# Kernel tuning notes

Hardware: AMD Instinct MI355X
Metric: run time of the kernel (lower is better)

The kernel has to match this reference:

```python
import jax, jax.numpy as jnp
import numpy as np

C, C_LO, C_MF = 96, 32, 32  # c_hf = 96 - 32 - 32 = 32
K_LO, K_HI, LP_FINE, LP_COARSE = 5, 3, 3, 7
BN_EPS = 1e-5


def _avgpool_same(x, k):
    """AvgPool2d(k, stride=1, padding=k//2, count_include_pad=False) on NCHW."""
    p = k // 2
    dims, strides = (1, 1, k, k), (1, 1, 1, 1)
    pads = ((0, 0), (0, 0), (p, p), (p, p))
    s = jax.lax.reduce_window(x, jnp.float32(0), jax.lax.add, dims, strides, pads)
    ones = jnp.ones((1, 1) + x.shape[2:], x.dtype)
    cnt = jax.lax.reduce_window(ones, jnp.float32(0), jax.lax.add, dims, strides, pads)
    return s / cnt  # divide by number of VALID (non-pad) elements


def _dwconv(x, w, k):
    """Depthwise conv, 'same' padding, no bias. w: (C, 1, k, k)."""
    p = k // 2
    return jax.lax.conv_general_dilated(
        x, w, window_strides=(1, 1), padding=((p, p), (p, p)),
        dimension_numbers=("NCHW", "OIHW", "NCHW"),
        feature_group_count=x.shape[1])


def setup_inputs() -> dict:
    key = jax.random.key(0)
    ks = jax.random.split(key, 8)
    B, H, W = 8, 256, 256
    return {
        "x": jax.random.normal(ks[0], (B, C, H, W), jnp.float32),
        "w_lo": jax.random.normal(ks[1], (C_LO, 1, K_LO, K_LO), jnp.float32) * 0.1,
        "w_mf": jax.random.normal(ks[2], (C_MF, 1, 3, 3), jnp.float32) * 0.2,
        "w_hf": jax.random.normal(ks[3], (C - C_LO - C_MF, 1, K_HI, K_HI), jnp.float32) * 0.2,
        "bn_gamma": jax.random.uniform(ks[4], (C,), jnp.float32, 0.5, 1.5),
        "bn_beta": jax.random.normal(ks[5], (C,), jnp.float32) * 0.1,
        "bn_mean": jax.random.normal(ks[6], (C,), jnp.float32) * 0.1,
        "bn_var": jax.random.uniform(ks[7], (C,), jnp.float32, 0.5, 1.5),
    }


def reference(x, w_lo, w_mf, w_hf, bn_gamma, bn_beta, bn_mean, bn_var):
    x_lo = x[:, :C_LO]
    x_mf = x[:, C_LO:C_LO + C_MF]
    x_hf = x[:, C_LO + C_MF:]

    y_lo = _dwconv(x_lo, w_lo, K_LO)
    # band-pass: fine low-pass minus coarse low-pass
    x_mf_bp = _avgpool_same(x_mf, LP_FINE) - _avgpool_same(x_mf, LP_COARSE)
    y_mf = _dwconv(x_mf_bp, w_mf, 3)
    # high-pass: identity minus fine low-pass
    x_hf_hp = x_hf - _avgpool_same(x_hf, LP_FINE)
    y_hf = _dwconv(x_hf_hp, w_hf, K_HI)

    y = jnp.concatenate([y_lo, y_mf, y_hf], axis=1)

    # channel shuffle with groups=3 (C % 3 == 0 here)
    B, Cc, H, W = y.shape
    y = y.reshape(B, 3, Cc // 3, H, W).transpose(0, 2, 1, 3, 4).reshape(B, Cc, H, W)

    # BatchNorm2d (inference mode, running stats) + SiLU
    inv = bn_gamma * jax.lax.rsqrt(bn_var + BN_EPS)
    y = y * inv[None, :, None, None] + (bn_beta - bn_mean * inv)[None, :, None, None]
    return jax.nn.silu(y)
```

## Files before the change

kernel.cpp:

```cpp
#include <hip/hip_runtime.h>

#define HH 256
#define WW 256
#define CC 96
#define BB 8

__device__ __forceinline__ float silu_of(float z) {
    return z / (1.0f + __expf(-z));
}

__global__ __launch_bounds__(256, 4)
void trifreq_kernel(const float* __restrict__ x,
                    const float* __restrict__ w_lo,
                    const float* __restrict__ w_mf,
                    const float* __restrict__ w_hf,
                    const float* __restrict__ gamma,
                    const float* __restrict__ beta,
                    const float* __restrict__ mean,
                    const float* __restrict__ var,
                    float* __restrict__ out)
{
    __shared__ __align__(16) float xs[74 * 72 + 16];
    __shared__ __align__(16) float tmp[36 * 68];

    const int tid = threadIdx.x;
    const int tileIdx = blockIdx.x;
    const int c = blockIdx.y;
    const int b = blockIdx.z;
    const int th = (tileIdx >> 2) * 64;
    const int tw = (tileIdx & 3) * 64;

    const int g = c >> 5;
    const int ci = c & 31;
    const int c_out = ci * 3 + g;

    const float* __restrict__ xin = x + (((size_t)b * CC + c) * (size_t)HH) * (size_t)WW;

    for (int idx = tid; idx < 72 * 18; idx += 256) {
        const int r  = idx / 18;
        const int c4 = idx % 18;
        const int gh = th - 4 + r;
        const int gw = tw - 4 + 4 * c4;
        float4 v = make_float4(0.f, 0.f, 0.f, 0.f);
        if (gh >= 0 && gh < HH && gw >= 0 && gw + 3 < WW) {
            v = *reinterpret_cast<const float4*>(xin + (size_t)gh * WW + gw);
        }
        *reinterpret_cast<float4*>(&xs[r * 72 + 4 * c4]) = v;
    }
    __syncthreads();

    if (g == 0) {
        const int qr = (tid >> 4) << 2;
        const int qc = (tid & 15) << 2;
        const float* __restrict__ wp = w_lo + ci * 25;
        float wk[25];
        #pragma unroll
        for (int t = 0; t < 25; ++t) wk[t] = wp[t];
        float acc[4][4];
        #pragma unroll
        for (int i = 0; i < 4; ++i)
            #pragma unroll
            for (int j = 0; j < 4; ++j) acc[i][j] = 0.f;

        #pragma unroll
        for (int rr = 0; rr < 8; ++rr) {
            const float* row = &xs[(qr + rr + 2) * 72 + qc];
            float v[12];
            *reinterpret_cast<float4*>(&v[0]) = *reinterpret_cast<const float4*>(row);
            *reinterpret_cast<float4*>(&v[4]) = *reinterpret_cast<const float4*>(row + 4);
            *reinterpret_cast<float4*>(&v[8]) = *reinterpret_cast<const float4*>(row + 8);
            #pragma unroll
            for (int i = 0; i < 4; ++i) {
                const int ki = rr - i;
                if (ki >= 0 && ki < 5) {
                    #pragma unroll
                    for (int j = 0; j < 4; ++j)
                        acc[i][j] += v[j + 2] * wk[ki * 5 + 0]
                                   + v[j + 3] * wk[ki * 5 + 1]
                                   + v[j + 4] * wk[ki * 5 + 2]
                                   + v[j + 5] * wk[ki * 5 + 3]
                                   + v[j + 6] * wk[ki * 5 + 4];
                }
            }
        }

        const float bninv  = gamma[c_out] * rsqrtf(var[c_out] + 1e-5f);
        const float bnbias = beta[c_out] - mean[c_out] * bninv;
        float* __restrict__ op = out + (((size_t)b * CC + c_out) * (size_t)HH + (th + qr)) * (size_t)WW + (tw + qc);
        #pragma unroll
        for (int i = 0; i < 4; ++i) {
            float4 o;
            o.x = silu_of(acc[i][0] * bninv + bnbias);
            o.y = silu_of(acc[i][1] * bninv + bnbias);
            o.z = silu_of(acc[i][2] * bninv + bnbias);
            o.w = silu_of(acc[i][3] * bninv + bnbias);
            *reinterpret_cast<float4*>(op + (size_t)i * WW) = o;
        }
    } else {
        for (int c0 = 0; c0 < 2; ++c0) {
            const int R0 = c0 * 32 - 1;

            if (tid < 153) {
                int pr, pc;
                if (tid < 144) { pr = tid >> 4; pc = tid & 15; }
                else           { pr = tid - 144; pc = 16; }
                const int bc = pc * 4 - 1;
                const int hb = th + R0 + pr * 4;
                const int wb = tw + bc;

                if (g == 1) {
                    const int xrb = R0 + 1 + pr * 4;
                    float v7a[4][4] = {};
                    float v3a[4][4] = {};
                    #pragma unroll
                    for (int rr = 0; rr < 10; ++rr) {
                        const float* row = &xs[(xrb + rr) * 72 + pc * 4];
                        float v[12];
                        *reinterpret_cast<float4*>(&v[0]) = *reinterpret_cast<const float4*>(row);
                        *reinterpret_cast<float4*>(&v[4]) = *reinterpret_cast<const float4*>(row + 4);
                        *reinterpret_cast<float4*>(&v[8]) = *reinterpret_cast<const float4*>(row + 8);
                        float h7[4], h3[4];
                        float s = v[0] + v[1] + v[2] + v[3] + v[4] + v[5] + v[6];
                        h7[0] = s;
                        h7[1] = h7[0] + v[7] - v[0];
                        h7[2] = h7[1] + v[8] - v[1];
                        h7[3] = h7[2] + v[9] - v[2];
                        #pragma unroll
                        for (int j = 0; j < 4; ++j) h3[j] = v[j + 2] + v[j + 3] + v[j + 4];
                        #pragma unroll
                        for (int k = 0; k < 4; ++k) {
                            if (rr >= k && rr <= k + 6) {
                                #pragma unroll
                                for (int j = 0; j < 4; ++j) v7a[k][j] += h7[j];
                            }
                            if (rr >= k + 2 && rr <= k + 4) {
                                #pragma unroll
                                for (int j = 0; j < 4; ++j) v3a[k][j] += h3[j];
                            }
                        }
                    }
                    float r3h[4], r7h[4], r3w[4], r7w[4];
                    if (hb >= 3 && hb + 6 <= HH - 1) {
                        #pragma unroll
                        for (int i = 0; i < 4; ++i) { r3h[i] = (1.f / 3.f); r7h[i] = (1.f / 7.f); }
                    } else {
                        #pragma unroll
                        for (int i = 0; i < 4; ++i) {
                            const int hh = hb + i;
                            const int a3 = min(hh + 1, HH - 1) - max(hh - 1, 0) + 1;
                            const int a7 = min(hh + 3, HH - 1) - max(hh - 3, 0) + 1;
                            r3h[i] = 1.0f / (float)a3;
                            r7h[i] = 1.0f / (float)a7;
                        }
                    }
                    if (wb >= 3 && wb + 6 <= WW - 1) {
                        #pragma unroll
                        for (int j = 0; j < 4; ++j) { r3w[j] = (1.f / 3.f); r7w[j] = (1.f / 7.f); }
                    } else {
                        #pragma unroll
                        for (int j = 0; j < 4; ++j) {
                            const int ww = wb + j;
                            const int a3 = min(ww + 1, WW - 1) - max(ww - 1, 0) + 1;
                            const int a7 = min(ww + 3, WW - 1) - max(ww - 3, 0) + 1;
                            r3w[j] = 1.0f / (float)a3;
                            r7w[j] = 1.0f / (float)a7;
                        }
                    }
                    #pragma unroll
                    for (int i = 0; i < 4; ++i) {
                        const int hh = hb + i;
                        float bpv[4];
                        #pragma unroll
                        for (int j = 0; j < 4; ++j) {
                            const int ww = wb + j;
                            float bp = 0.f;
                            if (hh >= 0 && hh < HH && ww >= 0 && ww < WW)
                                bp = v3a[i][j] * (r3h[i] * r3w[j]) - v7a[i][j] * (r7h[i] * r7w[j]);
                            bpv[j] = bp;
                        }
                        *reinterpret_cast<float4*>(&tmp[(pr * 4 + i) * 68 + pc * 4]) =
                            make_float4(bpv[0], bpv[1], bpv[2], bpv[3]);
                    }
                } else {
                    const int xrb = R0 + 3 + pr * 4;
                    float v3a[4][4] = {};
                    float cen[4][4];
                    #pragma unroll
                    for (int rr = 0; rr < 6; ++rr) {
                        const float* row = &xs[(xrb + rr) * 72 + pc * 4];
                        float v[8];
                        *reinterpret_cast<float4*>(&v[0]) = *reinterpret_cast<const float4*>(row);
                        *reinterpret_cast<float4*>(&v[4]) = *reinterpret_cast<const float4*>(row + 4);
                        float h3[4];
                        #pragma unroll
                        for (int j = 0; j < 4; ++j) h3[j] = v[j + 2] + v[j + 3] + v[j + 4];
                        if (rr >= 1 && rr <= 4) {
                            #pragma unroll
                            for (int j = 0; j < 4; ++j) cen[rr - 1][j] = v[j + 3];
                        }
                        #pragma unroll
                        for (int k = 0; k < 4; ++k) {
                            if (rr >= k && rr <= k + 2) {
                                #pragma unroll
                                for (int j = 0; j < 4; ++j) v3a[k][j] += h3[j];
                            }
                        }
                    }
                    float r3h[4], r3w[4];
                    if (hb >= 1 && hb + 4 <= HH - 1) {
                        #pragma unroll
                        for (int i = 0; i < 4; ++i) r3h[i] = (1.f / 3.f);
                    } else {
                        #pragma unroll
                        for (int i = 0; i < 4; ++i) {
                            const int hh = hb + i;
                            const int a3 = min(hh + 1, HH - 1) - max(hh - 1, 0) + 1;
                            r3h[i] = 1.0f / (float)a3;
                        }
                    }
                    if (wb >= 1 && wb + 4 <= WW - 1) {
                        #pragma unroll
                        for (int j = 0; j < 4; ++j) r3w[j] = (1.f / 3.f);
                    } else {
                        #pragma unroll
                        for (int j = 0; j < 4; ++j) {
                            const int ww = wb + j;
                            const int a3 = min(ww + 1, WW - 1) - max(ww - 1, 0) + 1;
                            r3w[j] = 1.0f / (float)a3;
                        }
                    }
                    #pragma unroll
                    for (int i = 0; i < 4; ++i) {
                        const int hh = hb + i;
                        float hpv[4];
                        #pragma unroll
                        for (int j = 0; j < 4; ++j) {
                            const int ww = wb + j;
                            float hp = 0.f;
                            if (hh >= 0 && hh < HH && ww >= 0 && ww < WW)
                                hp = cen[i][j] - v3a[i][j] * (r3h[i] * r3w[j]);
                            hpv[j] = hp;
                        }
                        *reinterpret_cast<float4*>(&tmp[(pr * 4 + i) * 68 + pc * 4]) =
                            make_float4(hpv[0], hpv[1], hpv[2], hpv[3]);
                    }
                }
            }
            __syncthreads();

            const float* __restrict__ wp = ((g == 1) ? w_mf : w_hf) + ci * 9;
            float wk[9];
            #pragma unroll
            for (int t = 0; t < 9; ++t) wk[t] = wp[t];

            const int lqr = (tid >> 4) * 2;
            const int qc  = (tid & 15) * 4;
            float acc2[2][4];
            #pragma unroll
            for (int i = 0; i < 2; ++i)
                #pragma unroll
                for (int j = 0; j < 4; ++j) acc2[i][j] = 0.f;

            #pragma unroll
            for (int rr = 0; rr < 4; ++rr) {
                const float* row = &tmp[(lqr + rr) * 68 + qc];
                float v[8];
                *reinterpret_cast<float4*>(&v[0]) = *reinterpret_cast<const float4*>(row);
                *reinterpret_cast<float4*>(&v[4]) = *reinterpret_cast<const float4*>(row + 4);
                #pragma unroll
                for (int i = 0; i < 2; ++i) {
                    const int ki = rr - i;
                    if (ki >= 0 && ki < 3) {
                        #pragma unroll
                        for (int j = 0; j < 4; ++j)
                            acc2[i][j] += v[j + 0] * wk[ki * 3 + 0]
                                        + v[j + 1] * wk[ki * 3 + 1]
                                        + v[j + 2] * wk[ki * 3 + 2];
                    }
                }
            }

            const float bninv  = gamma[c_out] * rsqrtf(var[c_out] + 1e-5f);
            const float bnbias = beta[c_out] - mean[c_out] * bninv;
            float* __restrict__ op = out + (((size_t)b * CC + c_out) * (size_t)HH
                                            + (th + c0 * 32 + lqr)) * (size_t)WW + (tw + qc);
            #pragma unroll
            for (int i = 0; i < 2; ++i) {
                float4 o;
                o.x = silu_of(acc2[i][0] * bninv + bnbias);
                o.y = silu_of(acc2[i][1] * bninv + bnbias);
                o.z = silu_of(acc2[i][2] * bninv + bnbias);
                o.w = silu_of(acc2[i][3] * bninv + bnbias);
                *reinterpret_cast<float4*>(op + (size_t)i * WW) = o;
            }

            if (c0 == 0) __syncthreads();
        }
    }
}

extern "C" void kernel_launch(void* const* d_in, const int* in_sizes, int n_in,
                              void* d_out, int out_size, void* d_ws, size_t ws_size,
                              hipStream_t stream) {
    const float* x     = (const float*)d_in[0];
    const float* w_lo  = (const float*)d_in[1];
    const float* w_mf  = (const float*)d_in[2];
    const float* w_hf  = (const float*)d_in[3];
    const float* gam   = (const float*)d_in[4];
    const float* bet   = (const float*)d_in[5];
    const float* mea   = (const float*)d_in[6];
    const float* va    = (const float*)d_in[7];
    float* out = (float*)d_out;

    dim3 grid(16, CC, BB);
    dim3 block(256);
    hipLaunchKernelGGL(trifreq_kernel, grid, block, 0, stream,
                       x, w_lo, w_mf, w_hf, gam, bet, mea, va, out);
}
```

Measured before the change: 420.1 us.

## Store filtered intermediate tile as fp16 and process full 64-row tile in one pass

The band-pass and high-pass intermediate tile is now stored in shared memory as half precision. The saved space allows the whole 66x66 prefilter region to be held at once, so the two half-tile passes with their extra barrier and halo recomputation are replaced by a single pass. The 3x3 conv and the BN+SiLU epilogue are unified with the low-band path using 4x4 outputs per thread. The fp16 rounding of intermediates adds numerical error, and the prefilter loop is now strided over 289 work items.

```diff
diff --git a/kernel.cpp b/kernel.cpp
--- a/kernel.cpp
+++ b/kernel.cpp
@@ -1,4 +1,5 @@
 #include <hip/hip_runtime.h>
+#include <hip/hip_fp16.h>
 
 #define HH 256
 #define WW 256
@@ -21,7 +22,7 @@
                     float* __restrict__ out)
 {
     __shared__ __align__(16) float xs[74 * 72 + 16];
-    __shared__ __align__(16) float tmp[36 * 68];
+    __shared__ __align__(16) __half tmp[68 * 68 + 8];
 
     const int tid = threadIdx.x;
     const int tileIdx = blockIdx.x;
@@ -49,14 +50,15 @@
     }
     __syncthreads();
 
+    const int qr = (tid >> 4) << 2;
+    const int qc = (tid & 15) << 2;
+    float acc[4][4];
+
     if (g == 0) {
-        const int qr = (tid >> 4) << 2;
-        const int qc = (tid & 15) << 2;
         const float* __restrict__ wp = w_lo + ci * 25;
         float wk[25];
         #pragma unroll
         for (int t = 0; t < 25; ++t) wk[t] = wp[t];
-        float acc[4][4];
         #pragma unroll
         for (int i = 0; i < 4; ++i)
             #pragma unroll
@@ -83,219 +85,200 @@
                 }
             }
         }
-
-        const float bninv  = gamma[c_out] * rsqrtf(var[c_out] + 1e-5f);
-        const float bnbias = beta[c_out] - mean[c_out] * bninv;
-        float* __restrict__ op = out + (((size_t)b * CC + c_out) * (size_t)HH + (th + qr)) * (size_t)WW + (tw + qc);
-        #pragma unroll
-        for (int i = 0; i < 4; ++i) {
-            float4 o;
-            o.x = silu_of(acc[i][0] * bninv + bnbias);
-            o.y = silu_of(acc[i][1] * bninv + bnbias);
-            o.z = silu_of(acc[i][2] * bninv + bnbias);
-            o.w = silu_of(acc[i][3] * bninv + bnbias);
-            *reinterpret_cast<float4*>(op + (size_t)i * WW) = o;
-        }
     } else {
-        for (int c0 = 0; c0 < 2; ++c0) {
-            const int R0 = c0 * 32 - 1;
-
-            if (tid < 153) {
-                int pr, pc;
-                if (tid < 144) { pr = tid >> 4; pc = tid & 15; }
-                else           { pr = tid - 144; pc = 16; }
-                const int bc = pc * 4 - 1;
-                const int hb = th + R0 + pr * 4;
+        if (g == 1) {
+            for (int p = tid; p < 17 * 17; p += 256) {
+                const int pr = p / 17, pc = p % 17;
+                const int br = pr * 4 - 1, bc = pc * 4 - 1;
+                const int hb = th + br;
                 const int wb = tw + bc;
-
-                if (g == 1) {
-                    const int xrb = R0 + 1 + pr * 4;
-                    float v7a[4][4] = {};
-                    float v3a[4][4] = {};
-                    #pragma unroll
-                    for (int rr = 0; rr < 10; ++rr) {
-                        const float* row = &xs[(xrb + rr) * 72 + pc * 4];
-                        float v[12];
-                        *reinterpret_cast<float4*>(&v[0]) = *reinterpret_cast<const float4*>(row);
-                        *reinterpret_cast<float4*>(&v[4]) = *reinterpret_cast<const float4*>(row + 4);
-                        *reinterpret_cast<float4*>(&v[8]) = *reinterpret_cast<const float4*>(row + 8);
-                        float h7[4], h3[4];
-                        float s = v[0] + v[1] + v[2] + v[3] + v[4] + v[5] + v[6];
-                        h7[0] = s;
-                        h7[1] = h7[0] + v[7] - v[0];
-                        h7[2] = h7[1] + v[8] - v[1];
-                        h7[3] = h7[2] + v[9] - v[2];
-                        #pragma unroll
-                        for (int j = 0; j < 4; ++j) h3[j] = v[j + 2] + v[j + 3] + v[j + 4];
-                        #pragma unroll
-                        for (int k = 0; k < 4; ++k) {
-                            if (rr >= k && rr <= k + 6) {
-                                #pragma unroll
-                                for (int j = 0; j < 4; ++j) v7a[k][j] += h7[j];
-                            }
-                            if (rr >= k + 2 && rr <= k + 4) {
-                                #pragma unroll
-                                for (int j = 0; j < 4; ++j) v3a[k][j] += h3[j];
-                            }
+                float v7a[4][4] = {};
+                float v3a[4][4] = {};
+                #pragma unroll
+                for (int rr = 0; rr < 10; ++rr) {
+                    const float* row = &xs[(pr * 4 + rr) * 72 + pc * 4];
+                    float v[12];
+                    *reinterpret_cast<float4*>(&v[0]) = *reinterpret_cast<const float4*>(row);
+                    *reinterpret_cast<float4*>(&v[4]) = *reinterpret_cast<const float4*>(row + 4);
+                    *reinterpret_cast<float4*>(&v[8]) = *reinterpret_cast<const float4*>(row + 8);
+                    float h7[4], h3[4];
+                    float s = v[0] + v[1] + v[2] + v[3] + v[4] + v[5] + v[6];
+                    h7[0] = s;
+                    h7[1] = h7[0] + v[7] - v[0];
+                    h7[2] = h7[1] + v[8] - v[1];
+                    h7[3] = h7[2] + v[9] - v[2];
+                    #pragma unroll
+                    for (int j = 0; j < 4; ++j) h3[j] = v[j + 2] + v[j + 3] + v[j + 4];
+                    #pragma unroll
+                    for (int k = 0; k < 4; ++k) {
+                        if (rr >= k && rr <= k + 6) {
+                            #pragma unroll
+                            for (int j = 0; j < 4; ++j) v7a[k][j] += h7[j];
                         }
-                    }
-                    float r3h[4], r7h[4], r3w[4], r7w[4];
-                    if (hb >= 3 && hb + 6 <= HH - 1) {
-                        #pragma unroll
-                        for (int i = 0; i < 4; ++i) { r3h[i] = (1.f / 3.f); r7h[i] = (1.f / 7.f); }
-                    } else {
-                        #pragma unroll
-                        for (int i = 0; i < 4; ++i) {
-                            const int hh = hb + i;
-                            const int a3 = min(hh + 1, HH - 1) - max(hh - 1, 0) + 1;
-                            const int a7 = min(hh + 3, HH - 1) - max(hh - 3, 0) + 1;
-                            r3h[i] = 1.0f / (float)a3;
-                            r7h[i] = 1.0f / (float)a7;
+                        if (rr >= k + 2 && rr <= k + 4) {
+                            #pragma unroll
+                            for (int j = 0; j < 4; ++j) v3a[k][j] += h3[j];
                         }
                     }
-                    if (wb >= 3 && wb + 6 <= WW - 1) {
-                        #pragma unroll
-                        for (int j = 0; j < 4; ++j) { r3w[j] = (1.f / 3.f); r7w[j] = (1.f / 7.f); }
-                    } else {
-                        #pragma unroll
-                        for (int j = 0; j < 4; ++j) {
-                            const int ww = wb + j;
-                            const int a3 = min(ww + 1, WW - 1) - max(ww - 1, 0) + 1;
-                            const int a7 = min(ww + 3, WW - 1) - max(ww - 3, 0) + 1;
-                            r3w[j] = 1.0f / (float)a3;
-                            r7w[j] = 1.0f / (float)a7;
-                        }
-                    }
+                }
+                float r3h[4], r7h[4], r3w[4], r7w[4];
+                if (hb >= 3 && hb + 6 <= HH - 1) {
+                    #pragma unroll
+                    for (int i = 0; i < 4; ++i) { r3h[i] = (1.f / 3.f); r7h[i] = (1.f / 7.f); }
+                } else {
                     #pragma unroll
                     for (int i = 0; i < 4; ++i) {
                         const int hh = hb + i;
-                        float bpv[4];
+                        const int a3 = min(hh + 1, HH - 1) - max(hh - 1, 0) + 1;
+                        const int a7 = min(hh + 3, HH - 1) - max(hh - 3, 0) + 1;
+                        r3h[i] = 1.0f / (float)a3;
+                        r7h[i] = 1.0f / (float)a7;
+                    }
+                }
+                if (wb >= 3 && wb + 6 <= WW - 1) {
+                    #pragma unroll
+                    for (int j = 0; j < 4; ++j) { r3w[j] = (1.f / 3.f); r7w[j] = (1.f / 7.f); }
+                } else {
+                    #pragma unroll
+                    for (int j = 0; j < 4; ++j) {
+                        const int ww = wb + j;
+                        const int a3 = min(ww + 1, WW - 1) - max(ww - 1, 0) + 1;
+                        const int a7 = min(ww + 3, WW - 1) - max(ww - 3, 0) + 1;
+                        r3w[j] = 1.0f / (float)a3;
+                        r7w[j] = 1.0f / (float)a7;
+                    }
+                }
+                #pragma unroll
+                for (int i = 0; i < 4; ++i) {
+                    const int hh = hb + i;
+                    float bpv[4];
+                    #pragma unroll
+                    for (int j = 0; j < 4; ++j) {
+                        const int ww = wb + j;
+                        float bp = 0.f;
+                        if (hh >= 0 && hh < HH && ww >= 0 && ww < WW)
+                            bp = v3a[i][j] * (r3h[i] * r3w[j]) - v7a[i][j] * (r7h[i] * r7w[j]);
+                        bpv[j] = bp;
+                    }
+                    __half2* trow = reinterpret_cast<__half2*>(&tmp[(pr * 4 + i) * 68 + pc * 4]);
+                    trow[0] = __floats2half2_rn(bpv[0], bpv[1]);
+                    trow[1] = __floats2half2_rn(bpv[2], bpv[3]);
+                }
+            }
+        } else {
+            for (int p = tid; p < 17 * 17; p += 256) {
+                const int pr = p / 17, pc = p % 17;
+                const int br = pr * 4 - 1, bc = pc * 4 - 1;
+                const int hb = th + br;
+                const int wb = tw + bc;
+                float v3a[4][4] = {};
+                float cen[4][4];
+                #pragma unroll
+                for (int rr = 0; rr < 6; ++rr) {
+                    const float* row = &xs[(pr * 4 + 2 + rr) * 72 + pc * 4];
+                    float v[8];
+                    *reinterpret_cast<float4*>(&v[0]) = *reinterpret_cast<const float4*>(row);
+                    *reinterpret_cast<float4*>(&v[4]) = *reinterpret_cast<const float4*>(row + 4);
+                    float h3[4];
+                    #pragma unroll
+                    for (int j = 0; j < 4; ++j) h3[j] = v[j + 2] + v[j + 3] + v[j + 4];
+                    if (rr >= 1 && rr <= 4) {
                         #pragma unroll
-                        for (int j = 0; j < 4; ++j) {
-                            const int ww = wb + j;
-                            float bp = 0.f;
-                            if (hh >= 0 && hh < HH && ww >= 0 && ww < WW)
-                                bp = v3a[i][j] * (r3h[i] * r3w[j]) - v7a[i][j] * (r7h[i] * r7w[j]);
-                            bpv[j] = bp;
+                        for (int j = 0; j < 4; ++j) cen[rr - 1][j] = v[j + 3];
+                    }
+                    #pragma unroll
+                    for (int k = 0; k < 4; ++k) {
+                        if (rr >= k && rr <= k + 2) {
+                            #pragma unroll
+                            for (int j = 0; j < 4; ++j) v3a[k][j] += h3[j];
                         }
-                        *reinterpret_cast<float4*>(&tmp[(pr * 4 + i) * 68 + pc * 4]) =
-                            make_float4(bpv[0], bpv[1], bpv[2], bpv[3]);
-                    }
+                    }
+                }
+                float r3h[4], r3w[4];
+                if (hb >= 1 && hb + 4 <= HH - 1) {
+                    #pragma unroll
+                    for (int i = 0; i < 4; ++i) r3h[i] = (1.f / 3.f);
                 } else {
-                    const int xrb = R0 + 3 + pr * 4;
-                    float v3a[4][4] = {};
-                    float cen[4][4];
-                    #pragma unroll
-                    for (int rr = 0; rr < 6; ++rr) {
-                        const float* row = &xs[(xrb + rr) * 72 + pc * 4];
-                        float v[8];
-                        *reinterpret_cast<float4*>(&v[0]) = *reinterpret_cast<const float4*>(row);
-                        *reinterpret_cast<float4*>(&v[4]) = *reinterpret_cast<const float4*>(row + 4);
-                        float h3[4];
-                        #pragma unroll
-                        for (int j = 0; j < 4; ++j) h3[j] = v[j + 2] + v[j + 3] + v[j + 4];
-                        if (rr >= 1 && rr <= 4) {
-                            #pragma unroll
-                            for (int j = 0; j < 4; ++j) cen[rr - 1][j] = v[j + 3];
-                        }
-                        #pragma unroll
-                        for (int k = 0; k < 4; ++k) {
-                            if (rr >= k && rr <= k + 2) {
-                                #pragma unroll
-                                for (int j = 0; j < 4; ++j) v3a[k][j] += h3[j];
-                            }
-                        }
-                    }
-                    float r3h[4], r3w[4];
-                    if (hb >= 1 && hb + 4 <= HH - 1) {
-                        #pragma unroll
-                        for (int i = 0; i < 4; ++i) r3h[i] = (1.f / 3.f);
-                    } else {
-                        #pragma unroll
-                        for (int i = 0; i < 4; ++i) {
-                            const int hh = hb + i;
-                            const int a3 = min(hh + 1, HH - 1) - max(hh - 1, 0) + 1;
-                            r3h[i] = 1.0f / (float)a3;
-                        }
-                    }
-                    if (wb >= 1 && wb + 4 <= WW - 1) {
-                        #pragma unroll
-                        for (int j = 0; j < 4; ++j) r3w[j] = (1.f / 3.f);
-                    } else {
-                        #pragma unroll
-                        for (int j = 0; j < 4; ++j) {
-                            const int ww = wb + j;
-                            const int a3 = min(ww + 1, WW - 1) - max(ww - 1, 0) + 1;
-                            r3w[j] = 1.0f / (float)a3;
-                        }
-                    }
                     #pragma unroll
                     for (int i = 0; i < 4; ++i) {
                         const int hh = hb + i;
-                        float hpv[4];
-                        #pragma unroll
-                        for (int j = 0; j < 4; ++j) {
-                            const int ww = wb + j;
-                            float hp = 0.f;
-                            if (hh >= 0 && hh < HH && ww >= 0 && ww < WW)
-                                hp = cen[i][j] - v3a[i][j] * (r3h[i] * r3w[j]);
-                            hpv[j] = hp;
-                        }
-                        *reinterpret_cast<float4*>(&tmp[(pr * 4 + i) * 68 + pc * 4]) =
-                            make_float4(hpv[0], hpv[1], hpv[2], hpv[3]);
-                    }
+                        const int a3 = min(hh + 1, HH - 1) - max(hh - 1, 0) + 1;
+                        r3h[i] = 1.0f / (float)a3;
+                    }
+                }
+                if (wb >= 1 && wb + 4 <= WW - 1) {
+                    #pragma unroll
+                    for (int j = 0; j < 4; ++j) r3w[j] = (1.f / 3.f);
+                } else {
+                    #pragma unroll
+                    for (int j = 0; j < 4; ++j) {
+                        const int ww = wb + j;
+                        const int a3 = min(ww + 1, WW - 1) - max(ww - 1, 0) + 1;
+                        r3w[j] = 1.0f / (float)a3;
+                    }
+                }
+                #pragma unroll
+                for (int i = 0; i < 4; ++i) {
+                    const int hh = hb + i;
+                    float hpv[4];
+                    #pragma unroll
+                    for (int j = 0; j < 4; ++j) {
+                        const int ww = wb + j;
+                        float hp = 0.f;
+                        if (hh >= 0 && hh < HH && ww >= 0 && ww < WW)
+                            hp = cen[i][j] - v3a[i][j] * (r3h[i] * r3w[j]);
+                        hpv[j] = hp;
+                    }
+                    __half2* trow = reinterpret_cast<__half2*>(&tmp[(pr * 4 + i) * 68 + pc * 4]);
+                    trow[0] = __floats2half2_rn(hpv[0], hpv[1]);
+                    trow[1] = __floats2half2_rn(hpv[2], hpv[3]);
                 }
             }
-            __syncthreads();
-
-            const float* __restrict__ wp = ((g == 1) ? w_mf : w_hf) + ci * 9;
-            float wk[9];
+        }
+        __syncthreads();
+
+        const float* __restrict__ wp = ((g == 1) ? w_mf : w_hf) + ci * 9;
+        float wk[9];
+        #pragma unroll
+        for (int t = 0; t < 9; ++t) wk[t] = wp[t];
+        #pragma unroll
+        for (int i = 0; i < 4; ++i)
             #pragma unroll
-            for (int t = 0; t < 9; ++t) wk[t] = wp[t];
-
-            const int lqr = (tid >> 4) * 2;
-            const int qc  = (tid & 15) * 4;
-            float acc2[2][4];
+            for (int j = 0; j < 4; ++j) acc[i][j] = 0.f;
+
+        #pragma unroll
+        for (int rr = 0; rr < 6; ++rr) {
+            const __half2* hrow = reinterpret_cast<const __half2*>(&tmp[(qr + rr) * 68 + qc]);
+            const float2 va = __half22float2(hrow[0]);
+            const float2 vb = __half22float2(hrow[1]);
+            const float2 vc = __half22float2(hrow[2]);
+            float v[6];
+            v[0] = va.x; v[1] = va.y; v[2] = vb.x; v[3] = vb.y; v[4] = vc.x; v[5] = vc.y;
             #pragma unroll
-            for (int i = 0; i < 2; ++i)
-                #pragma unroll
-                for (int j = 0; j < 4; ++j) acc2[i][j] = 0.f;
-
-            #pragma unroll
-            for (int rr = 0; rr < 4; ++rr) {
-                const float* row = &tmp[(lqr + rr) * 68 + qc];
-                float v[8];
-                *reinterpret_cast<float4*>(&v[0]) = *reinterpret_cast<const float4*>(row);
-                *reinterpret_cast<float4*>(&v[4]) = *reinterpret_cast<const float4*>(row + 4);
-                #pragma unroll
-                for (int i = 0; i < 2; ++i) {
-                    const int ki = rr - i;
-                    if (ki >= 0 && ki < 3) {
-                        #pragma unroll
-                        for (int j = 0; j < 4; ++j)
-                            acc2[i][j] += v[j + 0] * wk[ki * 3 + 0]
-                                        + v[j + 1] * wk[ki * 3 + 1]
-                                        + v[j + 2] * wk[ki * 3 + 2];
-                    }
+            for (int i = 0; i < 4; ++i) {
+                const int ki = rr - i;
+                if (ki >= 0 && ki < 3) {
+                    #pragma unroll
+                    for (int j = 0; j < 4; ++j)
+                        acc[i][j] += v[j + 0] * wk[ki * 3 + 0]
+                                   + v[j + 1] * wk[ki * 3 + 1]
+                                   + v[j + 2] * wk[ki * 3 + 2];
                 }
             }
-
-            const float bninv  = gamma[c_out] * rsqrtf(var[c_out] + 1e-5f);
-            const float bnbias = beta[c_out] - mean[c_out] * bninv;
-            float* __restrict__ op = out + (((size_t)b * CC + c_out) * (size_t)HH
-                                            + (th + c0 * 32 + lqr)) * (size_t)WW + (tw + qc);
-            #pragma unroll
-            for (int i = 0; i < 2; ++i) {
-                float4 o;
-                o.x = silu_of(acc2[i][0] * bninv + bnbias);
-                o.y = silu_of(acc2[i][1] * bninv + bnbias);
-                o.z = silu_of(acc2[i][2] * bninv + bnbias);
-                o.w = silu_of(acc2[i][3] * bninv + bnbias);
-                *reinterpret_cast<float4*>(op + (size_t)i * WW) = o;
-            }
-
-            if (c0 == 0) __syncthreads();
         }
+    }
+
+    const float bninv  = gamma[c_out] * rsqrtf(var[c_out] + 1e-5f);
+    const float bnbias = beta[c_out] - mean[c_out] * bninv;
+    float* __restrict__ op = out + (((size_t)b * CC + c_out) * (size_t)HH + (th + qr)) * (size_t)WW + (tw + qc);
+    #pragma unroll
+    for (int i = 0; i < 4; ++i) {
+        float4 o;
+        o.x = silu_of(acc[i][0] * bninv + bnbias);
+        o.y = silu_of(acc[i][1] * bninv + bnbias);
+        o.z = silu_of(acc[i][2] * bninv + bnbias);
+        o.w = silu_of(acc[i][3] * bninv + bnbias);
+        *reinterpret_cast<float4*>(op + (size_t)i * WW) = o;
     }
 }
 
```

Result: no change. 416.3 us (-0.9%).
